# Performance work log

Measured on AMD Instinct MI355X. Metric: run time of the kernel, lower is better.

Reference implementation:

```python
import jax, jax.numpy as jnp
import numpy as np

N1, C, T1, V = 16, 64, 512, 25
NH, DK, DV, BD = 8, 64, 64, 64
DKH, DVH = DK // NH, DV // NH
NB = T1 // BD


def rel_to_abs(x):
    # x: (..., L, 2L-1) -> (..., L, L)  (rel-shift trick)
    *lead, L, _ = x.shape
    x = jnp.pad(x, [(0, 0)] * (x.ndim - 1) + [(0, 1)])      # (..., L, 2L)
    x = x.reshape(*lead, L * 2 * L)
    x = jnp.pad(x, [(0, 0)] * (x.ndim - 1) + [(0, L - 1)])
    x = x.reshape(*lead, L + 1, 2 * L - 1)
    return x[..., :L, L - 1:]


def setup_inputs() -> dict:
    key = jax.random.key(0)
    ks = jax.random.split(key, 6)
    return {
        "x": jax.random.normal(ks[0], (N1, C, T1, V), jnp.float32),
        "w_qkv": jax.random.normal(ks[1], (2 * DK + DV, C), jnp.float32) * 0.05,
        "b_qkv": jax.random.normal(ks[2], (2 * DK + DV,), jnp.float32) * 0.01,
        "w_out": jax.random.normal(ks[3], (DV, DV), jnp.float32) * 0.05,
        "b_out": jax.random.normal(ks[4], (DV,), jnp.float32) * 0.01,
        "key_rel": jax.random.normal(ks[5], (2 * BD - 1, DKH), jnp.float32),
    }


def reference(x, w_qkv, b_qkv, w_out, b_out, key_rel):
    B = N1 * V
    # (N1,C,T1,V) -> (N1*V, C, T1); 1x1 qkv conv == GEMM over channels
    xr = x.transpose(0, 3, 1, 2).reshape(B, C, T1)
    qkv = jnp.einsum('oc,bct->bot', w_qkv, xr) + b_qkv[None, :, None]
    q, k, v = qkv[:, :DK], qkv[:, DK:2 * DK], qkv[:, 2 * DK:]
    # split heads and blocks: (B, NH, dh, NB, BD); all blocks vectorized
    q = q.reshape(B, NH, DKH, NB, BD) * (DKH ** -0.5)
    k = k.reshape(B, NH, DKH, NB, BD)
    v = v.reshape(B, NH, DVH, NB, BD)
    logits = jnp.einsum('bhdnt,bhdns->bhnts', q, k)          # (B,NH,NB,BD,BD)
    # relative position logits (rel-shift)
    qb = q.transpose(0, 1, 3, 4, 2)                          # (B,NH,NB,BD,DKH)
    rel = jnp.einsum('bhntd,md->bhntm', qb, key_rel)         # (B,NH,NB,BD,2BD-1)
    logits = logits + rel_to_abs(rel)
    weights = jax.nn.softmax(logits, axis=-1)
    out = jnp.einsum('bhnts,bhdns->bhdnt', weights, v)       # (B,NH,DVH,NB,BD)
    # combine heads (head-major channels) and blocks along T
    out = out.reshape(B, DV, T1)
    ao = jnp.einsum('oc,bct->bot', w_out, out) + b_out[None, :, None]
    ao = ao.reshape(N1, V, DV, T1).transpose(0, 2, 3, 1)     # (N1,DV,T1,V)
    return jax.nn.relu(ao + x)
```

## Files before the change

### kernel.cpp

```cpp
#include <hip/hip_runtime.h>
#include <math.h>

#define Vc 25
#define QSCALE 0.35355339059327373f

typedef short bf16x8 __attribute__((ext_vector_type(8), may_alias));
typedef short bf16x4 __attribute__((ext_vector_type(4), may_alias));
typedef unsigned int u32a __attribute__((may_alias));
typedef float f32x4 __attribute__((ext_vector_type(4)));

#define FENCE() asm volatile("" ::: "memory")

#define WQA_O 0
#define BQ_O  12288
#define KRT_O 12672
#define WOA_O 13760

__device__ __forceinline__ unsigned short f2bf(float f) {
    unsigned u = __builtin_bit_cast(unsigned, f);
    u = (u + 0x7fff + ((u >> 16) & 1)) >> 16;
    return (unsigned short)u;
}
__device__ __forceinline__ float bf2f(unsigned short h) {
    unsigned u = ((unsigned)h) << 16;
    return __builtin_bit_cast(float, u);
}

__global__ void prep_kernel(const float* __restrict__ w_qkv, const float* __restrict__ b_qkv,
                            const float* __restrict__ w_out, const float* __restrict__ key_rel,
                            unsigned short* __restrict__ ws)
{
    const int gid = blockIdx.x * 256 + threadIdx.x;
    const int gsz = gridDim.x * 256;
    for (int id = gid; id < 12288; id += gsz) {
        int j = id & 7, lane = (id >> 3) & 63, ks = (id >> 9) & 1, mt = id >> 10;
        int m = mt * 16 + (lane & 15);
        int k = ks * 32 + (lane >> 4) * 8 + j;
        ws[WQA_O + id] = f2bf(w_qkv[m * 64 + k] * (m < 64 ? QSCALE : 1.f));
    }
    float* bq = (float*)(ws + BQ_O);
    for (int id = gid; id < 192; id += gsz)
        bq[id] = b_qkv[id] * (id < 64 ? QSCALE : 1.f);
    for (int id = gid; id < 1088; id += gsz) {
        int d = id & 7, m = id >> 3;
        ws[KRT_O + id] = (m < 127) ? f2bf(key_rel[m * 8 + d]) : (unsigned short)0;
    }
    for (int id = gid; id < 4096; id += gsz) {
        int j = id & 7, lane = (id >> 3) & 63, mtg = id >> 9;
        int m = (mtg & 3) * 16 + (lane & 15);
        int k = (mtg >> 2) * 32 + (lane >> 4) * 8 + j;
        ws[WOA_O + id] = f2bf(w_out[m * 64 + k]);
    }
}

#define QT_O   0
#define KT_O   4160
#define VS_O   8320
#define OT_O   12992
#define SCR_O  15552
#define SMEM_U16 21952

__global__ __launch_bounds__(256, 3)
void tcn_attn(const float* __restrict__ x, const float* __restrict__ b_out,
              const unsigned short* __restrict__ ws, float* __restrict__ y)
{
    __shared__ unsigned short sm[SMEM_U16];

    const int tid  = threadIdx.x;
    const int lane = tid & 63;
    const int w    = tid >> 6;
    const int li   = lane & 15;
    const int lq   = lane >> 4;
    const int koff = lq * 8;
    const int n    = blockIdx.x;
    const int b    = blockIdx.y;
    const int n1   = b / Vc;
    const int v    = b - n1 * Vc;
    const int t0   = n * 64;
    const int trow = 16 * w + li;
    const unsigned scr = SCR_O + w * 1600;

    const bf16x8 z8 = {0,0,0,0,0,0,0,0};
    const f32x4  z4 = {0.f,0.f,0.f,0.f};

    for (int i = tid; i < 7776; i += 256)
        ((u32a*)sm)[i] = 0u;

    float xres[16];
    f32x4 pacc[4];
    #pragma unroll
    for (int mt = 0; mt < 4; ++mt)
        #pragma unroll
        for (int r = 0; r < 4; ++r) {
            int o = mt * 16 + lq * 4 + r;
            xres[mt * 4 + r] = x[((n1 * 64 + o) * 512 + t0 + 16 * w + li) * Vc + v];
            pacc[mt][r] = b_out[o];
        }

    #pragma unroll
    for (int i = 0; i < 16; ++i) {
        int e = tid + 256 * i, t = e & 63, c = e >> 6;
        sm[SCR_O + t * 72 + c] = f2bf(x[((n1 * 64 + c) * 512 + t0 + t) * Vc + v]);
    }
    __syncthreads();

    const unsigned short* wq = ws + WQA_O;
    const float* bq = (const float*)(ws + BQ_O);
    #pragma unroll
    for (int sec = 0; sec < 3; ++sec) {
        const int mt = sec * 4 + w;
        bf16x8 a0 = *(const bf16x8*)(wq + ((mt * 2 + 0) * 64 + lane) * 8);
        bf16x8 a1 = *(const bf16x8*)(wq + ((mt * 2 + 1) * 64 + lane) * 8);
        f32x4 acc[4];
        #pragma unroll
        for (int nt = 0; nt < 4; ++nt) {
            #pragma unroll
            for (int r = 0; r < 4; ++r) acc[nt][r] = bq[mt * 16 + lq * 4 + r];
            bf16x8 b0 = *(const bf16x8*)(sm + SCR_O + (16 * nt + li) * 72 + koff);
            bf16x8 b1 = *(const bf16x8*)(sm + SCR_O + (16 * nt + li) * 72 + 32 + koff);
            acc[nt] = __builtin_amdgcn_mfma_f32_16x16x32_bf16(a0, b0, acc[nt], 0, 0, 0);
            acc[nt] = __builtin_amdgcn_mfma_f32_16x16x32_bf16(a1, b1, acc[nt], 0, 0, 0);
        }
        const int h2 = 2 * w + (lq >> 1);
        if (sec < 2) {
            const unsigned base = (sec == 0 ? QT_O : KT_O) + h2 * 520 + (lq & 1) * 4;
            #pragma unroll
            for (int nt = 0; nt < 4; ++nt) {
                bf16x4 p;
                p.x = (short)f2bf(acc[nt][0]);
                p.y = (short)f2bf(acc[nt][1]);
                p.z = (short)f2bf(acc[nt][2]);
                p.w = (short)f2bf(acc[nt][3]);
                *(bf16x4*)(sm + base + (16 * nt + li) * 8) = p;
            }
        } else {
            #pragma unroll
            for (int nt = 0; nt < 4; ++nt)
                #pragma unroll
                for (int r = 0; r < 4; ++r)
                    sm[VS_O + h2 * 584 + ((lq & 1) * 4 + r) * 72 + 16 * nt + li] = f2bf(acc[nt][r]);
        }
    }
    __syncthreads();

    bf16x8 br[5];
    #pragma unroll
    for (int j = 0; j < 5; ++j)
        br[j] = *(const bf16x8*)(ws + KRT_O + (16 * (3 - w + j) + li) * 8 + koff);

    for (int h = 0; h < 8; ++h) {
        bf16x8 aq = *(const bf16x8*)(sm + QT_O + h * 520 + trow * 8 + koff);
        if (lane >= 16) aq = z8;

        f32x4 qk[4];
        #pragma unroll
        for (int nt = 0; nt < 4; ++nt) {
            bf16x8 bk = *(const bf16x8*)(sm + KT_O + h * 520 + (16 * nt + li) * 8 + koff);
            qk[nt] = __builtin_amdgcn_mfma_f32_16x16x32_bf16(aq, bk, z4, 0, 0, 0);
        }
        #pragma unroll
        for (int j = 0; j < 5; ++j) {
            f32x4 rl = __builtin_amdgcn_mfma_f32_16x16x32_bf16(aq, br[j], z4, 0, 0, 0);
            bf16x4 p;
            p.x = (short)f2bf(rl[0]);
            p.y = (short)f2bf(rl[1]);
            p.z = (short)f2bf(rl[2]);
            p.w = (short)f2bf(rl[3]);
            *(bf16x4*)(sm + scr + (16 * j + li) * 20 + 4 * lq) = p;
        }
        FENCE();
        float ex[4][4], lsum[4] = {0.f, 0.f, 0.f, 0.f};
        #pragma unroll
        for (int nt = 0; nt < 4; ++nt)
            #pragma unroll
            for (int r = 0; r < 4; ++r) {
                int mp = 16 * nt + li - 4 * lq - r + 15;
                float rv = bf2f(sm[scr + mp * 20 + 4 * lq + r]);
                float e = __expf(qk[nt][r] + rv);
                ex[nt][r] = e;
                lsum[r] += e;
            }
        FENCE();
        float linv[4];
        #pragma unroll
        for (int r = 0; r < 4; ++r) {
            float s = lsum[r];
            s += __shfl_xor(s, 1);
            s += __shfl_xor(s, 2);
            s += __shfl_xor(s, 4);
            s += __shfl_xor(s, 8);
            linv[r] = 1.0f / s;
        }
        #pragma unroll
        for (int nt = 0; nt < 4; ++nt)
            #pragma unroll
            for (int r = 0; r < 4; ++r)
                sm[scr + (4 * lq + r) * 72 + 16 * nt + li] = f2bf(ex[nt][r] * linv[r]);
        FENCE();
        f32x4 av = z4;
        #pragma unroll
        for (int ks = 0; ks < 2; ++ks) {
            bf16x8 aa = *(const bf16x8*)(sm + scr + li * 72 + ks * 32 + koff);
            bf16x8 bv = *(const bf16x8*)(sm + VS_O + h * 584 + (li & 7) * 72 + ks * 32 + koff);
            av = __builtin_amdgcn_mfma_f32_16x16x32_bf16(aa, bv, av, 0, 0, 0);
        }
        if (li < 8) {
            #pragma unroll
            for (int r = 0; r < 4; ++r)
                sm[OT_O + (16 * w + 4 * lq + r) * 40 + (h & 3) * 8 + li] = f2bf(av[r]);
        }
        if ((h & 3) == 3) {
            FENCE();
            bf16x8 bo = *(const bf16x8*)(sm + OT_O + trow * 40 + koff);
            const int g = h >> 2;
            #pragma unroll
            for (int mt = 0; mt < 4; ++mt) {
                bf16x8 ao = *(const bf16x8*)(ws + WOA_O + ((g * 4 + mt) * 64 + lane) * 8);
                pacc[mt] = __builtin_amdgcn_mfma_f32_16x16x32_bf16(ao, bo, pacc[mt], 0, 0, 0);
            }
        }
        FENCE();
    }

    #pragma unroll
    for (int mt = 0; mt < 4; ++mt)
        #pragma unroll
        for (int r = 0; r < 4; ++r) {
            int o = mt * 16 + lq * 4 + r;
            int idx = ((n1 * 64 + o) * 512 + t0 + 16 * w + li) * Vc + v;
            y[idx] = fmaxf(pacc[mt][r] + xres[mt * 4 + r], 0.f);
        }
}

extern "C" void kernel_launch(void* const* d_in, const int* in_sizes, int n_in,
                              void* d_out, int out_size, void* d_ws, size_t ws_size,
                              hipStream_t stream) {
    const float* x       = (const float*)d_in[0];
    const float* w_qkv   = (const float*)d_in[1];
    const float* b_qkv   = (const float*)d_in[2];
    const float* w_out   = (const float*)d_in[3];
    const float* b_out   = (const float*)d_in[4];
    const float* key_rel = (const float*)d_in[5];
    float* y = (float*)d_out;
    unsigned short* ws = (unsigned short*)d_ws;

    prep_kernel<<<dim3(96), dim3(256), 0, stream>>>(w_qkv, b_qkv, w_out, key_rel, ws);
    dim3 grid(512 / 64, 400);
    tcn_attn<<<grid, dim3(256), 0, stream>>>(x, b_out, ws, y);
}
```

Measured before the change: 239.7 us.

## Software-pipeline head loop, defer softmax normalization, use DPP reductions and cheap bf16 packing

Fully unrolls the per-head loop and issues the next head's QK and relative-position MFMAs before the current head's softmax, so matrix work overlaps the exp and LDS traffic. Softmax normalization moves from the probabilities to the 16-wide attention output, and the row sums use DPP adds in place of shuffles. The bf16 conversion switches to round-half-up with perm-based packing, and LDS is zeroed with wider stores. This adds register pressure from the doubled qk/rl fragments and changes rounding slightly.

```diff
diff --git a/kernel.cpp b/kernel.cpp
--- a/kernel.cpp
+++ b/kernel.cpp
@@ -5,26 +5,48 @@
 #define QSCALE 0.35355339059327373f
 
 typedef short bf16x8 __attribute__((ext_vector_type(8), may_alias));
-typedef short bf16x4 __attribute__((ext_vector_type(4), may_alias));
-typedef unsigned int u32a __attribute__((may_alias));
+typedef unsigned int u32x2a __attribute__((ext_vector_type(2), may_alias));
 typedef float f32x4 __attribute__((ext_vector_type(4)));
 
 #define FENCE() asm volatile("" ::: "memory")
+
+__device__ __forceinline__ unsigned short f2bf(float f) {
+    unsigned u = __builtin_bit_cast(unsigned, f);
+    u = (u + 0x7fff + ((u >> 16) & 1)) >> 16;
+    return (unsigned short)u;
+}
+__device__ __forceinline__ unsigned short f2bf_fast(float f) {
+    unsigned u = __builtin_bit_cast(unsigned, f) + 0x8000u;
+    return (unsigned short)(u >> 16);
+}
+__device__ __forceinline__ unsigned pkbf(float lo, float hi) {
+    unsigned a = __builtin_bit_cast(unsigned, lo) + 0x8000u;
+    unsigned b = __builtin_bit_cast(unsigned, hi) + 0x8000u;
+    return __builtin_amdgcn_perm(b, a, 0x07060302);
+}
+__device__ __forceinline__ float bf2f(unsigned short h) {
+    unsigned u = ((unsigned)h) << 16;
+    return __builtin_bit_cast(float, u);
+}
+
+template<int CTRL>
+__device__ __forceinline__ float dpp_add(float x) {
+    int xi = __builtin_bit_cast(int, x);
+    int yi = __builtin_amdgcn_update_dpp(0, xi, CTRL, 0xf, 0xf, true);
+    return x + __builtin_bit_cast(float, yi);
+}
+__device__ __forceinline__ float row_sum16(float s) {
+    s = dpp_add<0xB1>(s);
+    s = dpp_add<0x4E>(s);
+    s = dpp_add<0x141>(s);
+    s = dpp_add<0x140>(s);
+    return s;
+}
 
 #define WQA_O 0
 #define BQ_O  12288
 #define KRT_O 12672
 #define WOA_O 13760
-
-__device__ __forceinline__ unsigned short f2bf(float f) {
-    unsigned u = __builtin_bit_cast(unsigned, f);
-    u = (u + 0x7fff + ((u >> 16) & 1)) >> 16;
-    return (unsigned short)u;
-}
-__device__ __forceinline__ float bf2f(unsigned short h) {
-    unsigned u = ((unsigned)h) << 16;
-    return __builtin_bit_cast(float, u);
-}
 
 __global__ void prep_kernel(const float* __restrict__ w_qkv, const float* __restrict__ b_qkv,
                             const float* __restrict__ w_out, const float* __restrict__ key_rel,
@@ -83,8 +105,8 @@
     const bf16x8 z8 = {0,0,0,0,0,0,0,0};
     const f32x4  z4 = {0.f,0.f,0.f,0.f};
 
-    for (int i = tid; i < 7776; i += 256)
-        ((u32a*)sm)[i] = 0u;
+    for (int i = tid; i < 1944; i += 256)
+        *(bf16x8*)(sm + i * 8) = z8;
 
     float xres[16];
     f32x4 pacc[4];
@@ -100,7 +122,7 @@
     #pragma unroll
     for (int i = 0; i < 16; ++i) {
         int e = tid + 256 * i, t = e & 63, c = e >> 6;
-        sm[SCR_O + t * 72 + c] = f2bf(x[((n1 * 64 + c) * 512 + t0 + t) * Vc + v]);
+        sm[SCR_O + t * 72 + c] = f2bf_fast(x[((n1 * 64 + c) * 512 + t0 + t) * Vc + v]);
     }
     __syncthreads();
 
@@ -126,19 +148,17 @@
             const unsigned base = (sec == 0 ? QT_O : KT_O) + h2 * 520 + (lq & 1) * 4;
             #pragma unroll
             for (int nt = 0; nt < 4; ++nt) {
-                bf16x4 p;
-                p.x = (short)f2bf(acc[nt][0]);
-                p.y = (short)f2bf(acc[nt][1]);
-                p.z = (short)f2bf(acc[nt][2]);
-                p.w = (short)f2bf(acc[nt][3]);
-                *(bf16x4*)(sm + base + (16 * nt + li) * 8) = p;
+                u32x2a p;
+                p.x = pkbf(acc[nt][0], acc[nt][1]);
+                p.y = pkbf(acc[nt][2], acc[nt][3]);
+                *(u32x2a*)(sm + base + (16 * nt + li) * 8) = p;
             }
         } else {
             #pragma unroll
             for (int nt = 0; nt < 4; ++nt)
                 #pragma unroll
                 for (int r = 0; r < 4; ++r)
-                    sm[VS_O + h2 * 584 + ((lq & 1) * 4 + r) * 72 + 16 * nt + li] = f2bf(acc[nt][r]);
+                    sm[VS_O + h2 * 584 + ((lq & 1) * 4 + r) * 72 + 16 * nt + li] = f2bf_fast(acc[nt][r]);
         }
     }
     __syncthreads();
@@ -148,25 +168,39 @@
     for (int j = 0; j < 5; ++j)
         br[j] = *(const bf16x8*)(ws + KRT_O + (16 * (3 - w + j) + li) * 8 + koff);
 
-    for (int h = 0; h < 8; ++h) {
+    auto FRONT = [&](int h, f32x4* qk, f32x4* rl) {
         bf16x8 aq = *(const bf16x8*)(sm + QT_O + h * 520 + trow * 8 + koff);
         if (lane >= 16) aq = z8;
-
-        f32x4 qk[4];
         #pragma unroll
         for (int nt = 0; nt < 4; ++nt) {
             bf16x8 bk = *(const bf16x8*)(sm + KT_O + h * 520 + (16 * nt + li) * 8 + koff);
             qk[nt] = __builtin_amdgcn_mfma_f32_16x16x32_bf16(aq, bk, z4, 0, 0, 0);
         }
         #pragma unroll
+        for (int j = 0; j < 5; ++j)
+            rl[j] = __builtin_amdgcn_mfma_f32_16x16x32_bf16(aq, br[j], z4, 0, 0, 0);
+    };
+
+    f32x4 qk[4], rl[5];
+    FRONT(0, qk, rl);
+
+    #pragma unroll
+    for (int h = 0; h < 8; ++h) {
+        #pragma unroll
         for (int j = 0; j < 5; ++j) {
-            f32x4 rl = __builtin_amdgcn_mfma_f32_16x16x32_bf16(aq, br[j], z4, 0, 0, 0);
-            bf16x4 p;
-            p.x = (short)f2bf(rl[0]);
-            p.y = (short)f2bf(rl[1]);
-            p.z = (short)f2bf(rl[2]);
-            p.w = (short)f2bf(rl[3]);
-            *(bf16x4*)(sm + scr + (16 * j + li) * 20 + 4 * lq) = p;
+            u32x2a p;
+            p.x = pkbf(rl[j][0], rl[j][1]);
+            p.y = pkbf(rl[j][2], rl[j][3]);
+            *(u32x2a*)(sm + scr + (16 * j + li) * 20 + 4 * lq) = p;
+        }
+        f32x4 qkn[4], rln[5];
+        if (h < 7) FRONT(h + 1, qkn, rln);
+        bf16x8 ao[4];
+        if ((h & 3) == 3) {
+            const int g = h >> 2;
+            #pragma unroll
+            for (int mt = 0; mt < 4; ++mt)
+                ao[mt] = *(const bf16x8*)(ws + WOA_O + ((g * 4 + mt) * 64 + lane) * 8);
         }
         FENCE();
         float ex[4][4], lsum[4] = {0.f, 0.f, 0.f, 0.f};
@@ -183,19 +217,13 @@
         FENCE();
         float linv[4];
         #pragma unroll
-        for (int r = 0; r < 4; ++r) {
-            float s = lsum[r];
-            s += __shfl_xor(s, 1);
-            s += __shfl_xor(s, 2);
-            s += __shfl_xor(s, 4);
-            s += __shfl_xor(s, 8);
-            linv[r] = 1.0f / s;
-        }
+        for (int r = 0; r < 4; ++r)
+            linv[r] = 1.0f / row_sum16(lsum[r]);
         #pragma unroll
         for (int nt = 0; nt < 4; ++nt)
             #pragma unroll
             for (int r = 0; r < 4; ++r)
-                sm[scr + (4 * lq + r) * 72 + 16 * nt + li] = f2bf(ex[nt][r] * linv[r]);
+                sm[scr + (4 * lq + r) * 72 + 16 * nt + li] = f2bf_fast(ex[nt][r]);
         FENCE();
         f32x4 av = z4;
         #pragma unroll
@@ -207,19 +235,22 @@
         if (li < 8) {
             #pragma unroll
             for (int r = 0; r < 4; ++r)
-                sm[OT_O + (16 * w + 4 * lq + r) * 40 + (h & 3) * 8 + li] = f2bf(av[r]);
+                sm[OT_O + (16 * w + 4 * lq + r) * 40 + (h & 3) * 8 + li] = f2bf_fast(av[r] * linv[r]);
         }
         if ((h & 3) == 3) {
             FENCE();
             bf16x8 bo = *(const bf16x8*)(sm + OT_O + trow * 40 + koff);
-            const int g = h >> 2;
-            #pragma unroll
-            for (int mt = 0; mt < 4; ++mt) {
-                bf16x8 ao = *(const bf16x8*)(ws + WOA_O + ((g * 4 + mt) * 64 + lane) * 8);
-                pacc[mt] = __builtin_amdgcn_mfma_f32_16x16x32_bf16(ao, bo, pacc[mt], 0, 0, 0);
-            }
-        }
-        FENCE();
+            #pragma unroll
+            for (int mt = 0; mt < 4; ++mt)
+                pacc[mt] = __builtin_amdgcn_mfma_f32_16x16x32_bf16(ao[mt], bo, pacc[mt], 0, 0, 0);
+        }
+        FENCE();
+        if (h < 7) {
+            #pragma unroll
+            for (int i = 0; i < 4; ++i) qk[i] = qkn[i];
+            #pragma unroll
+            for (int j = 0; j < 5; ++j) rl[j] = rln[j];
+        }
     }
 
     #pragma unroll
```

Measured after the change: 229.2 us. 1.05x faster.
